# Kernel tuning notes

Hardware: AMD Instinct MI355X
Metric: run time of the kernel (lower is better)

## Reference

```python
import jax, jax.numpy as jnp
import numpy as np

N_ATOMS = 512
HEADS = 3
D1 = 16   # embedding_size1
D2 = 8    # embedding_size2
L1 = 32   # linear_size1
L2 = 16   # linear_size2
EPS = 1e-5


def _bn(x, gamma, beta):
    # PyG BatchNorm in training mode: batch statistics over nodes
    mu = x.mean(0)
    var = x.var(0)
    return (x - mu) * jax.lax.rsqrt(var + EPS) * gamma + beta


def setup_inputs() -> dict:
    key = jax.random.key(0)
    ks = jax.random.split(key, 24)
    N, E, C_in, C_out = 131072, 2097152, 32, 64
    s = lambda k, shape, fan: jax.random.normal(k, shape, jnp.float32) * (1.0 / np.sqrt(fan))
    inp = {
        "x": jax.random.normal(ks[0], (N, C_in), jnp.float32),
        "edge_index": jax.random.randint(ks[1], (2, E), 0, N, jnp.int64),
        # GATConv(in, 16, heads=3)
        "W_gat": s(ks[2], (C_in, HEADS * D1), C_in),
        "att_src": s(ks[3], (HEADS, D1), D1),
        "att_dst": s(ks[4], (HEADS, D1), D1),
        "b_gat": jnp.zeros((HEADS * D1,), jnp.float32),
        # head_transform1: Linear(48, 16)
        "W_ht": s(ks[5], (HEADS * D1, D1), HEADS * D1),
        "b_ht": jnp.zeros((D1,), jnp.float32),
        "g1": jnp.ones((D1,), jnp.float32),
        "be1": jnp.zeros((D1,), jnp.float32),
        # GCNConv(16, 8)
        "W_gcn": s(ks[6], (D1, D2), D1),
        "b_gcn": jnp.zeros((D2,), jnp.float32),
        "g2": jnp.ones((D2,), jnp.float32),
        "be2": jnp.zeros((D2,), jnp.float32),
        # dense head
        "W1": s(ks[7], (D2 * N_ATOMS, L1), D2 * N_ATOMS),
        "b1": jnp.zeros((L1,), jnp.float32),
        "W2": s(ks[8], (L1, L2), L1),
        "b2": jnp.zeros((L2,), jnp.float32),
        "Wt": s(ks[9], (L2, C_out), L2),
        "bt": jnp.zeros((C_out,), jnp.float32),
        "Wmu": s(ks[10], (C_out, C_out), C_out),
        "bmu": jnp.zeros((C_out,), jnp.float32),
        "Wls": s(ks[11], (C_out, C_out), C_out),
        "bls": jnp.zeros((C_out,), jnp.float32),
    }
    return inp


def _forward(x, edge_index, W_gat, att_src, att_dst, b_gat, W_ht, b_ht, g1, be1,
             W_gcn, b_gcn, g2, be2, W1, b1, W2, b2, Wt, bt, Wmu, bmu, Wls, bls):
    N = x.shape[0]
    loop = jnp.arange(N, dtype=edge_index.dtype)
    ei = jnp.concatenate([edge_index, jnp.stack([loop, loop])], axis=1)  # add self loops
    src, dst = ei[0], ei[1]

    # --- GATConv(in_channels, 16, heads=3) ---
    h = (x @ W_gat).reshape(N, HEADS, D1)                    # [N,H,D1]
    a_src = (h * att_src).sum(-1)                            # [N,H]
    a_dst = (h * att_dst).sum(-1)                            # [N,H]
    e = jax.nn.leaky_relu(a_src[src] + a_dst[dst], 0.2)      # [E',H]
    m = jax.ops.segment_max(e, dst, num_segments=N)          # per-target softmax
    w = jnp.exp(e - m[dst])
    z = jax.ops.segment_sum(w, dst, num_segments=N)
    alpha = w / z[dst]                                       # self-loops => z > 0
    msg = h[src] * alpha[:, :, None]                         # [E',H,D1]
    out = jax.ops.segment_sum(msg, dst, num_segments=N)
    out = out.reshape(N, HEADS * D1) + b_gat                 # concat heads + bias

    # head transform + BN1
    out = _bn(out @ W_ht + b_ht, g1, be1)                    # [N,16]

    # --- GCNConv(16, 8) with symmetric normalization ---
    deg = jax.ops.segment_sum(jnp.ones_like(dst, jnp.float32), dst, num_segments=N)
    dinv = jax.lax.rsqrt(deg)                                # deg >= 1 (self loops)
    norm = dinv[src] * dinv[dst]                             # [E']
    xw = out @ W_gcn                                         # [N,8]
    out = jax.ops.segment_sum(xw[src] * norm[:, None], dst, num_segments=N) + b_gcn
    out = _bn(out, g2, be2)                                  # [N,8]

    # --- per-graph dense head ---
    B = N // N_ATOMS
    out = out.reshape(B, N_ATOMS * D2)                       # flatten each graph
    out = jax.nn.leaky_relu(out @ W1 + b1)                   # [B,32]
    out = jax.nn.leaky_relu(out @ W2 + b2)                   # [B,16]
    out = jax.nn.leaky_relu(out @ Wt + bt)                   # [B,out]
    mu = out @ Wmu + bmu
    logstd = out @ Wls + bls
    return mu, logstd


def reference(x, edge_index, W_gat, att_src, att_dst, b_gat, W_ht, b_ht, g1, be1,
              W_gcn, b_gcn, g2, be2, W1, b1, W2, b2, Wt, bt, Wmu, bmu, Wls, bls):
    return _forward(x, edge_index, W_gat, att_src, att_dst, b_gat, W_ht, b_ht, g1, be1,
                    W_gcn, b_gcn, g2, be2, W1, b1, W2, b2, Wt, bt, Wmu, bmu, Wls, bls)
```

## Files before the change

### kernel.cpp

```cpp
#include <hip/hip_runtime.h>
#include <hip/hip_bf16.h>
#include <cstddef>

#define TPB 256
#define TPB_BIN 1024
#define NPB 512
#define BSH 9
#define CHUNK 8192

typedef unsigned int u32;

__device__ __forceinline__ float lrelu(float v, float s){ return v > 0.f ? v : s*v; }

__device__ __forceinline__ unsigned short bf16_rne(float f){
    u32 u = __float_as_uint(f);
    u += 0x7FFFu + ((u >> 16) & 1u);
    return (unsigned short)(u >> 16);
}
__device__ __forceinline__ float bf_lo(u32 w){ return __uint_as_float(w << 16); }
__device__ __forceinline__ float bf_hi(u32 w){ return __uint_as_float(w & 0xFFFF0000u); }

__global__ __launch_bounds__(TPB) void k1_embed(
    const float* __restrict__ x, const float* __restrict__ Wg,
    const float* __restrict__ atts, const float* __restrict__ attd,
    u32* __restrict__ hrow, float4* __restrict__ a_dst4, int N)
{
    __shared__ float Ws[32*48];
    __shared__ float As[48], Ad[48];
    for (int i = threadIdx.x; i < 32*48; i += TPB) Ws[i] = Wg[i];
    if (threadIdx.x < 48){ As[threadIdx.x] = atts[threadIdx.x]; Ad[threadIdx.x] = attd[threadIdx.x]; }
    __syncthreads();
    int n = blockIdx.x*TPB + threadIdx.x;
    if (n >= N) return;
    float xr[32];
    const float4* xp = (const float4*)(x + (size_t)n*32);
    #pragma unroll
    for (int i=0;i<8;i++){ float4 v = xp[i]; xr[4*i+0]=v.x; xr[4*i+1]=v.y; xr[4*i+2]=v.z; xr[4*i+3]=v.w; }
    float hv[48];
    #pragma unroll 4
    for (int j=0;j<48;j++){
        float acc = 0.f;
        #pragma unroll
        for (int i=0;i<32;i++) acc = fmaf(xr[i], Ws[i*48+j], acc);
        hv[j] = acc;
    }
    float asv[3], adv[3];
    #pragma unroll
    for (int hh=0;hh<3;hh++){
        float s0=0.f, s1=0.f;
        #pragma unroll
        for (int d=0;d<16;d++){ s0 = fmaf(hv[hh*16+d], As[hh*16+d], s0); s1 = fmaf(hv[hh*16+d], Ad[hh*16+d], s1); }
        asv[hh]=s0; adv[hh]=s1;
    }
    u32 w[24];
    #pragma unroll
    for (int q=0;q<12;q++){
        w[2*q]   = (u32)bf16_rne(hv[4*q+0]) | ((u32)bf16_rne(hv[4*q+1]) << 16);
        w[2*q+1] = (u32)bf16_rne(hv[4*q+2]) | ((u32)bf16_rne(hv[4*q+3]) << 16);
    }
    uint4* hp4 = (uint4*)(hrow + (size_t)n*32);
    hp4[0] = make_uint4(__float_as_uint(asv[0]), __float_as_uint(asv[1]), __float_as_uint(asv[2]), 0u);
    #pragma unroll
    for (int i=0;i<6;i++) hp4[1+i] = make_uint4(w[4*i],w[4*i+1],w[4*i+2],w[4*i+3]);
    hp4[7] = make_uint4(0u,0u,0u,0u);
    a_dst4[n] = make_float4(adv[0],adv[1],adv[2],0.f);
}

__global__ __launch_bounds__(TPB_BIN) void k_bin1(
    const int* __restrict__ ei, u32* __restrict__ staging,
    int* __restrict__ chunk_off, int* __restrict__ chunk_cnt,
    int* __restrict__ btot_pad, int E)
{
    __shared__ uint2 stash[CHUNK];
    __shared__ int lcnt[256], lcur[256];
    int t = threadIdx.x;
    int blockStart = blockIdx.x * CHUNK;
    int len = E - blockStart; if (len > CHUNK) len = CHUNK; if (len < 0) len = 0;
    if (t < 256) lcnt[t] = 0;
    __syncthreads();
    for (int i = t; i < len; i += TPB_BIN){
        int s = ei[blockStart + i];
        int d = ei[E + blockStart + i];
        stash[i] = make_uint2((unsigned)s, (unsigned)d);
        atomicAdd(&lcnt[d >> BSH], 1);
    }
    __syncthreads();
    if (t < 256){
        int myc = lcnt[t];
        atomicAdd(&btot_pad[t*16], myc);
        chunk_cnt[blockIdx.x*256 + t] = myc;
    }
    __syncthreads();
    if (t < 64){
        int v0=lcnt[4*t+0], v1=lcnt[4*t+1], v2=lcnt[4*t+2], v3=lcnt[4*t+3];
        int s = v0+v1+v2+v3, tot = s;
        #pragma unroll
        for (int off=1; off<64; off<<=1){ int xch = __shfl_up(s, off); if (t >= off) s += xch; }
        int base = s - tot;
        lcur[4*t+0]=base; lcur[4*t+1]=base+v0; lcur[4*t+2]=base+v0+v1; lcur[4*t+3]=base+v0+v1+v2;
    }
    __syncthreads();
    if (t < 256) chunk_off[blockIdx.x*256 + t] = lcur[t];
    __syncthreads();
    for (int i = t; i < len; i += TPB_BIN){
        uint2 e = stash[i];
        int b = (int)(e.y >> BSH);
        int pos = atomicAdd(&lcur[b], 1);
        staging[blockStart + pos] = e.x | ((e.y & (NPB-1u)) << 17);
    }
}

__global__ __launch_bounds__(TPB_BIN) void k_bin2(
    const u32* __restrict__ staging,
    const int* __restrict__ chunk_off, const int* __restrict__ chunk_cnt,
    const int* __restrict__ btot_pad, int* __restrict__ rowptr, int* __restrict__ cnt_g,
    int* __restrict__ csr_src, int NCB)
{
    __shared__ int co[256], cl[256];
    __shared__ int lcnt[NPB], lcur[NPB];
    __shared__ int cbs;
    int b = blockIdx.x, t = threadIdx.x;
    if (t < 256){
        co[t] = (t < NCB) ? chunk_off[t*256 + b] : 0;
        cl[t] = (t < NCB) ? chunk_cnt[t*256 + b] : 0;
    }
    if (t < NPB) lcnt[t] = 0;
    if (t < 64){
        int s = 0;
        for (int i=t; i<b; i+=64) s += btot_pad[i*16];
        #pragma unroll
        for (int off=32; off; off>>=1) s += __shfl_xor(s, off);
        if (t == 0) cbs = s;
    }
    __syncthreads();
    int cb = cbs;
    int wv = t >> 6, lane = t & 63;
    for (int c = wv; c < NCB; c += 16){
        int len = cl[c];
        size_t base = (size_t)c*CHUNK + co[c];
        for (int i = lane; i < len; i += 64){
            u32 val = staging[base + i];
            atomicAdd(&lcnt[(val>>17)&(NPB-1u)], 1);
        }
    }
    __syncthreads();
    if (t < 64){
        int v[8]; int ss = 0;
        #pragma unroll
        for (int k=0;k<8;k++){ v[k] = lcnt[8*t+k]; ss += v[k]; }
        int tot = ss;
        #pragma unroll
        for (int off=1; off<64; off<<=1){ int xch = __shfl_up(ss, off); if (t >= off) ss += xch; }
        int base = ss - tot;
        #pragma unroll
        for (int k=0;k<8;k++){ lcur[8*t+k] = base; base += v[k]; }
    }
    __syncthreads();
    if (t < NPB){ rowptr[b*NPB + t] = cb + lcur[t]; cnt_g[b*NPB + t] = lcnt[t]; }
    __syncthreads();
    for (int c = wv; c < NCB; c += 16){
        int len = cl[c];
        size_t base = (size_t)c*CHUNK + co[c];
        for (int i = lane; i < len; i += 64){
            u32 val = staging[base + i];
            int node = (int)((val>>17)&(NPB-1u));
            int pos = atomicAdd(&lcur[node],1);
            csr_src[cb+pos] = (int)(val & 0x1FFFFu);
        }
    }
}

__global__ __launch_bounds__(TPB) void k_gat(
    const int* __restrict__ rowptr, const int* __restrict__ cnt, const int* __restrict__ csr_src,
    const u32* __restrict__ hrow, const float* __restrict__ a_dstf,
    const float* __restrict__ b_gat,
    const float* __restrict__ W_ht, const float* __restrict__ b_ht,
    float* __restrict__ out_ht, float* __restrict__ part, int N, int cpx)
{
    __shared__ float Wh[768];
    __shared__ float bg[48], bh[16];
    __shared__ float gl[4][52];
    __shared__ float ls2[4][16];
    for (int i=threadIdx.x;i<768;i+=TPB) Wh[i]=W_ht[i];
    if (threadIdx.x<48) bg[threadIdx.x]=b_gat[threadIdx.x];
    if (threadIdx.x<16) bh[threadIdx.x]=b_ht[threadIdx.x];
    __syncthreads();
    int bid = blockIdx.x;
    int bid2 = (bid & 7)*cpx + (bid >> 3);
    int lane = threadIdx.x & 63;
    int wv = threadIdx.x >> 6;
    int n = bid2*4 + wv;

    int g = lane>>4, q = lane&15;
    int hq = (q < 12) ? (q >> 2) : (q - 12);
    if (q == 15) hq = 0;
    bool is_msg = (q < 12);
    bool is_z   = (q >= 12 && q < 15);

    float adh   = a_dstf[(size_t)n*4 + hq];
    float asn_h = __uint_as_float(hrow[(size_t)n*32 + hq]);
    float wself = __expf(lrelu(asn_h + adh, 0.2f));

    int rs = rowptr[n];
    int deg = cnt[n];

    float4 acc = make_float4(0.f,0.f,0.f,0.f);
    float zacc = 0.f;

    for (int base = 0; base < deg; base += 64){
        int m = deg - base; if (m > 64) m = 64;
        int idx = csr_src[rs + base + (lane < m ? lane : 0)];
        int niter = (m + 15) >> 4;
        for (int i = 0; i < niter; i++){
            int jj = g + (i << 4);
            int s0=__shfl(idx,jj), s1=__shfl(idx,jj+4), s2=__shfl(idx,jj+8), s3=__shfl(idx,jj+12);
            const u32* p0 = hrow + (size_t)s0*32;
            const u32* p1 = hrow + (size_t)s1*32;
            const u32* p2 = hrow + (size_t)s2*32;
            const u32* p3 = hrow + (size_t)s3*32;
            float av0=__uint_as_float(p0[hq]);
            float av1=__uint_as_float(p1[hq]);
            float av2=__uint_as_float(p2[hq]);
            float av3=__uint_as_float(p3[hq]);
            uint2 r0,r1,r2,r3;
            if (is_msg){
                r0=*(const uint2*)(p0+4+2*q); r1=*(const uint2*)(p1+4+2*q);
                r2=*(const uint2*)(p2+4+2*q); r3=*(const uint2*)(p3+4+2*q);
            }
            float w0 = (jj      < m) ? __expf(lrelu(av0+adh,0.2f)) : 0.f;
            float w1 = (jj + 4  < m) ? __expf(lrelu(av1+adh,0.2f)) : 0.f;
            float w2 = (jj + 8  < m) ? __expf(lrelu(av2+adh,0.2f)) : 0.f;
            float w3 = (jj + 12 < m) ? __expf(lrelu(av3+adh,0.2f)) : 0.f;
            if (is_msg){
                acc.x=fmaf(w0,bf_lo(r0.x),acc.x); acc.y=fmaf(w0,bf_hi(r0.x),acc.y);
                acc.z=fmaf(w0,bf_lo(r0.y),acc.z); acc.w=fmaf(w0,bf_hi(r0.y),acc.w);
                acc.x=fmaf(w1,bf_lo(r1.x),acc.x); acc.y=fmaf(w1,bf_hi(r1.x),acc.y);
                acc.z=fmaf(w1,bf_lo(r1.y),acc.z); acc.w=fmaf(w1,bf_hi(r1.y),acc.w);
                acc.x=fmaf(w2,bf_lo(r2.x),acc.x); acc.y=fmaf(w2,bf_hi(r2.x),acc.y);
                acc.z=fmaf(w2,bf_lo(r2.y),acc.z); acc.w=fmaf(w2,bf_hi(r2.y),acc.w);
                acc.x=fmaf(w3,bf_lo(r3.x),acc.x); acc.y=fmaf(w3,bf_hi(r3.x),acc.y);
                acc.z=fmaf(w3,bf_lo(r3.y),acc.z); acc.w=fmaf(w3,bf_hi(r3.y),acc.w);
            } else if (is_z){
                zacc += (w0+w1)+(w2+w3);
            }
        }
    }

    #pragma unroll
    for (int off=16; off<64; off<<=1){
        acc.x += __shfl_xor(acc.x, off); acc.y += __shfl_xor(acc.y, off);
        acc.z += __shfl_xor(acc.z, off); acc.w += __shfl_xor(acc.w, off);
        zacc  += __shfl_xor(zacc,  off);
    }
    float z_mine = __shfl(zacc, 12 + hq) + wself;

    if (g==0 && q<12){
        uint2 hs = *(const uint2*)(hrow + (size_t)n*32 + 4 + 2*q);
        float inv = 1.f / z_mine;
        float4 gq;
        gq.x = (acc.x + wself*bf_lo(hs.x))*inv + bg[4*q+0];
        gq.y = (acc.y + wself*bf_hi(hs.x))*inv + bg[4*q+1];
        gq.z = (acc.z + wself*bf_lo(hs.y))*inv + bg[4*q+2];
        gq.w = (acc.w + wself*bf_hi(hs.y))*inv + bg[4*q+3];
        *(float4*)&gl[wv][4*q] = gq;
    }
    __syncthreads();
    int j16 = lane & 15, pr = lane >> 4;
    float oacc = 0.f;
    const float* gv = &gl[wv][pr*12];
    #pragma unroll
    for (int k=0;k<12;k++) oacc = fmaf(gv[k], Wh[(pr*12+k)*16 + j16], oacc);
    oacc += __shfl_xor(oacc, 16);
    oacc += __shfl_xor(oacc, 32);
    float oval = oacc + bh[j16];
    if (lane < 16){
        out_ht[(size_t)n*16 + lane] = oval;
        ls2[wv][lane] = oval;
    }
    __syncthreads();
    int t = threadIdx.x;
    if (t < 16){
        float s=0.f, qd=0.f;
        #pragma unroll
        for (int w2=0;w2<4;w2++){ float v=ls2[w2][t]; s+=v; qd+=v*v; }
        part[(size_t)bid*32 + t] = s;
        part[(size_t)bid*32 + 16 + t] = qd;
    }
}

__global__ __launch_bounds__(TPB) void k_bnmid16(const float* __restrict__ part, float* __restrict__ part2)
{
    __shared__ float ls[8][32];
    int t = threadIdx.x, b = blockIdx.x;
    int col = t & 31, grp = t >> 5;
    float s = 0.f;
    #pragma unroll
    for (int i=0;i<16;i++){ int r = b*128 + grp*16 + i; s += part[(size_t)r*32 + col]; }
    ls[grp][col] = s; __syncthreads();
    if (t < 32){
        float a = 0.f;
        #pragma unroll
        for (int g=0; g<8; g++) a += ls[g][t];
        part2[(size_t)b*32 + t] = a;
    }
}

__global__ __launch_bounds__(TPB) void k_bnfin16(const float* __restrict__ part2, float* __restrict__ bn, int NB)
{
    __shared__ float ls[8][32];
    int t = threadIdx.x, col = t & 31, grp = t >> 5;
    float s = 0.f;
    for (int r=grp; r<NB; r+=8) s += part2[(size_t)r*32+col];
    ls[grp][col] = s; __syncthreads();
    if (t < 32){
        float a = 0.f;
        #pragma unroll
        for (int g=0; g<8; g++) a += ls[g][t];
        bn[t] = a;
    }
}

__global__ __launch_bounds__(TPB) void k_bnmid8(const float* __restrict__ part, float* __restrict__ part2)
{
    __shared__ float ls[16][16];
    int t = threadIdx.x, b = blockIdx.x;
    int col = t & 15, grp = t >> 4;
    float s = 0.f;
    #pragma unroll
    for (int i=0;i<8;i++){ int r = b*128 + grp + 16*i; s += part[(size_t)r*16 + col]; }
    ls[grp][col] = s; __syncthreads();
    if (t < 16){
        float a = 0.f;
        #pragma unroll
        for (int g=0; g<16; g++) a += ls[g][t];
        part2[(size_t)b*16 + t] = a;
    }
}

__global__ __launch_bounds__(TPB) void k_bnfin8(const float* __restrict__ part2, float* __restrict__ bn, int NB)
{
    __shared__ float ls[16][16];
    int t = threadIdx.x, col = t & 15, grp = t >> 4;
    float s = 0.f;
    for (int r=grp; r<NB; r+=16) s += part2[(size_t)r*16+col];
    ls[grp][col] = s; __syncthreads();
    if (t < 16){
        float a = 0.f;
        #pragma unroll
        for (int g=0; g<16; g++) a += ls[g][t];
        bn[t] = a;
    }
}

__global__ __launch_bounds__(TPB) void k5_bn1_gcnmm(
    const float* __restrict__ out_ht, const float* __restrict__ bn,
    const float* __restrict__ g1, const float* __restrict__ be1,
    const float* __restrict__ W_gcn, const int* __restrict__ cnt,
    float* __restrict__ dinv, uint4* __restrict__ xws, int N)
{
    __shared__ float sc[16], sh[16], Wg[128];
    int t = threadIdx.x;
    if (t < 16){
        float mu  = bn[t]/(float)N;
        float var = bn[16+t]/(float)N - mu*mu;
        float s = rsqrtf(var+1e-5f)*g1[t];
        sc[t]=s; sh[t]=be1[t]-mu*s;
    }
    if (t < 128) Wg[t] = W_gcn[t];
    __syncthreads();
    int n = blockIdx.x*TPB + t;
    if (n >= N) return;
    float v[16];
    const float4* ip = (const float4*)(out_ht + (size_t)n*16);
    #pragma unroll
    for (int q=0;q<4;q++){
        float4 vv = ip[q];
        v[4*q+0]=vv.x*sc[4*q+0]+sh[4*q+0];
        v[4*q+1]=vv.y*sc[4*q+1]+sh[4*q+1];
        v[4*q+2]=vv.z*sc[4*q+2]+sh[4*q+2];
        v[4*q+3]=vv.w*sc[4*q+3]+sh[4*q+3];
    }
    float dv = rsqrtf((float)(cnt[n]+1));
    float o[8];
    #pragma unroll
    for (int k=0;k<8;k++){
        float acc=0.f;
        #pragma unroll
        for (int j=0;j<16;j++) acc = fmaf(v[j], Wg[j*8+k], acc);
        o[k]=acc*dv;
    }
    u32 w0 = (u32)bf16_rne(o[0]) | ((u32)bf16_rne(o[1])<<16);
    u32 w1 = (u32)bf16_rne(o[2]) | ((u32)bf16_rne(o[3])<<16);
    u32 w2 = (u32)bf16_rne(o[4]) | ((u32)bf16_rne(o[5])<<16);
    u32 w3 = (u32)bf16_rne(o[6]) | ((u32)bf16_rne(o[7])<<16);
    xws[n] = make_uint4(w0,w1,w2,w3);
    dinv[n] = dv;
}

__global__ __launch_bounds__(TPB) void k_gcn(
    const int* __restrict__ rowptr, const int* __restrict__ cnt, const int* __restrict__ csr_src,
    const float* __restrict__ dinv, const uint4* __restrict__ xws,
    const float* __restrict__ b_gcn, float* __restrict__ gout, float* __restrict__ part, int N, int cpx)
{
    __shared__ float ls[16][16];
    int bid = blockIdx.x;
    int bid2 = (bid & 7)*cpx + (bid >> 3);
    int t = threadIdx.x;
    int node = bid2*16 + (t >> 4);
    int sub  = t & 15;
    int grp  = t >> 4;
    float val[8];
    #pragma unroll
    for (int k=0;k<8;k++) val[k]=0.f;
    if (node < N){
        int rs = rowptr[node], re = rs + cnt[node];
        float a0=0.f,a1=0.f,a2=0.f,a3=0.f,a4=0.f,a5=0.f,a6=0.f,a7=0.f;
        for (int j=rs+sub; j<re; j+=16){
            int s = csr_src[j];
            uint4 r = xws[s];
            a0 += bf_lo(r.x); a1 += bf_hi(r.x);
            a2 += bf_lo(r.y); a3 += bf_hi(r.y);
            a4 += bf_lo(r.z); a5 += bf_hi(r.z);
            a6 += bf_lo(r.w); a7 += bf_hi(r.w);
        }
        #pragma unroll
        for (int off=1; off<16; off<<=1){
            a0 += __shfl_xor(a0, off); a1 += __shfl_xor(a1, off);
            a2 += __shfl_xor(a2, off); a3 += __shfl_xor(a3, off);
            a4 += __shfl_xor(a4, off); a5 += __shfl_xor(a5, off);
            a6 += __shfl_xor(a6, off); a7 += __shfl_xor(a7, off);
        }
        if (sub == 0){
            uint4 r = xws[node];
            a0 += bf_lo(r.x); a1 += bf_hi(r.x);
            a2 += bf_lo(r.y); a3 += bf_hi(r.y);
            a4 += bf_lo(r.z); a5 += bf_hi(r.z);
            a6 += bf_lo(r.w); a7 += bf_hi(r.w);
            float dd = dinv[node];
            val[0]=fmaf(dd,a0,b_gcn[0]); val[1]=fmaf(dd,a1,b_gcn[1]);
            val[2]=fmaf(dd,a2,b_gcn[2]); val[3]=fmaf(dd,a3,b_gcn[3]);
            val[4]=fmaf(dd,a4,b_gcn[4]); val[5]=fmaf(dd,a5,b_gcn[5]);
            val[6]=fmaf(dd,a6,b_gcn[6]); val[7]=fmaf(dd,a7,b_gcn[7]);
            float4* op = (float4*)(gout + (size_t)node*8);
            op[0] = make_float4(val[0],val[1],val[2],val[3]);
            op[1] = make_float4(val[4],val[5],val[6],val[7]);
        }
    }
    if (sub == 0){
        #pragma unroll
        for (int k=0;k<8;k++){ ls[grp][k] = val[k]; ls[grp][8+k] = val[k]*val[k]; }
    }
    __syncthreads();
    if (t < 16){
        float s = 0.f;
        #pragma unroll
        for (int g2=0; g2<16; g2++) s += ls[g2][t];
        part[(size_t)bid*16 + t] = s;
    }
}

__global__ __launch_bounds__(TPB) void k8_head(
    const float* __restrict__ gcn, const float* __restrict__ bn2,
    const float* __restrict__ g2, const float* __restrict__ be2,
    const float* __restrict__ W1, const float* __restrict__ b1,
    const float* __restrict__ W2, const float* __restrict__ b2,
    const float* __restrict__ Wt, const float* __restrict__ bt,
    const float* __restrict__ Wmu, const float* __restrict__ bmu,
    const float* __restrict__ Wls, const float* __restrict__ bls,
    float* __restrict__ out, int N, int B)
{
    __shared__ float v[4096];
    __shared__ float red[8][32];
    __shared__ float y1[32], y2[16], y3[64];
    int b = blockIdx.x, t = threadIdx.x;
    float sc[8], sh[8];
    #pragma unroll
    for (int k=0;k<8;k++){
        float mu  = bn2[k]/(float)N;
        float var = bn2[8+k]/(float)N - mu*mu;
        float s = rsqrtf(var+1e-5f)*g2[k];
        sc[k]=s; sh[k]=be2[k]-mu*s;
    }
    const float* src = gcn + (size_t)b*4096;
    for (int i=t;i<4096;i+=TPB){ int k=i&7; v[i]=src[i]*sc[k]+sh[k]; }
    __syncthreads();
    int j = t & 31, c = t >> 5;
    float p = 0.f;
    int base = c*512;
    for (int i=0;i<512;i++) p = fmaf(v[base+i], W1[(size_t)(base+i)*32+j], p);
    red[c][j] = p;
    __syncthreads();
    if (t < 32){
        float a = b1[t];
        #pragma unroll
        for (int cc=0;cc<8;cc++) a += red[cc][t];
        y1[t] = lrelu(a, 0.01f);
    }
    __syncthreads();
    if (t < 16){
        float a = b2[t];
        #pragma unroll
        for (int i=0;i<32;i++) a = fmaf(y1[i], W2[i*16+t], a);
        y2[t] = lrelu(a, 0.01f);
    }
    __syncthreads();
    if (t < 64){
        float a = bt[t];
        #pragma unroll
        for (int i=0;i<16;i++) a = fmaf(y2[i], Wt[i*64+t], a);
        y3[t] = lrelu(a, 0.01f);
    }
    __syncthreads();
    if (t < 64){
        float amu = bmu[t], als = bls[t];
        #pragma unroll
        for (int i=0;i<64;i++){ amu = fmaf(y3[i], Wmu[i*64+t], amu); als = fmaf(y3[i], Wls[i*64+t], als); }
        out[(size_t)b*64 + t] = amu;
        out[(size_t)B*64 + (size_t)b*64 + t] = als;
    }
}

extern "C" void kernel_launch(void* const* d_in, const int* in_sizes, int n_in,
                              void* d_out, int out_size, void* d_ws, size_t ws_size,
                              hipStream_t stream)
{
    const float* x     = (const float*)d_in[0];
    const int*   ei    = (const int*)  d_in[1];
    const float* W_gat = (const float*)d_in[2];
    const float* atts  = (const float*)d_in[3];
    const float* attd  = (const float*)d_in[4];
    const float* b_gat = (const float*)d_in[5];
    const float* W_ht  = (const float*)d_in[6];
    const float* b_ht  = (const float*)d_in[7];
    const float* g1    = (const float*)d_in[8];
    const float* be1   = (const float*)d_in[9];
    const float* W_gcn = (const float*)d_in[10];
    const float* b_gcn = (const float*)d_in[11];
    const float* g2    = (const float*)d_in[12];
    const float* be2   = (const float*)d_in[13];
    const float* W1    = (const float*)d_in[14];
    const float* b1    = (const float*)d_in[15];
    const float* W2    = (const float*)d_in[16];
    const float* b2    = (const float*)d_in[17];
    const float* Wt    = (const float*)d_in[18];
    const float* bt    = (const float*)d_in[19];
    const float* Wmu   = (const float*)d_in[20];
    const float* bmu   = (const float*)d_in[21];
    const float* Wls   = (const float*)d_in[22];
    const float* bls   = (const float*)d_in[23];
    float* out = (float*)d_out;

    const int N = in_sizes[0] / 32;
    const int E = in_sizes[1] / 2;
    const int B = N / 512;
    const int NBUCK = N / NPB;
    const int NCB = (E + CHUNK - 1) / CHUNK;

    char* wsb = (char*)d_ws;
    size_t off = 0;
    auto alloc = [&](size_t bytes){ void* p = wsb + off; off += (bytes + 255) & ~(size_t)255; return p; };
    char*   hreg    = (char*)  alloc((size_t)N*128);
    float*  out_ht  = (float*) alloc((size_t)N*16*4);
    float4* a_dst4  = (float4*)alloc((size_t)N*16);
    float*  dinv    = (float*) alloc((size_t)N*4);
    float*  bn      = (float*) alloc(64*4);
    int*    cnt     = (int*)   alloc((size_t)N*4);
    int*    rowptr  = (int*)   alloc((size_t)N*4);
    float*  part    = (float*) alloc((size_t)(N/4)*32*4);
    float*  part2   = (float*) alloc(8192*4);
    int*    csr_src = (int*)   alloc((size_t)E*4);
    u32*    staging = (u32*)   alloc((size_t)NCB*CHUNK*4);
    int*    chunk_off = (int*) alloc((size_t)NCB*256*4);
    int*    chunk_cnt = (int*) alloc((size_t)NCB*256*4);
    int*    btot_pad  = (int*) alloc((size_t)NBUCK*16*4);
    u32*    hrow    = (u32*)hreg;
    uint4*  xws     = (uint4*)hreg;
    float*  gout    = (float*)(hreg + (size_t)N*16);

    hipMemsetAsync(btot_pad, 0, (size_t)NBUCK*16*4, stream);

    dim3 tb(TPB);
    dim3 tbb(TPB_BIN);
    int gbN = (N+TPB-1)/TPB;
    int nbGat = N/4;
    int nbGcn = N/16;

    k_bin1   <<<NCB,   tbb, 0, stream>>>(ei, staging, chunk_off, chunk_cnt, btot_pad, E);
    k_bin2   <<<NBUCK, tbb, 0, stream>>>(staging, chunk_off, chunk_cnt, btot_pad, rowptr, cnt, csr_src, NCB);
    k1_embed <<<gbN,   tb, 0, stream>>>(x, W_gat, atts, attd, hrow, a_dst4, N);
    k_gat    <<<nbGat, tb, 0, stream>>>(rowptr, cnt, csr_src, hrow, (const float*)a_dst4,
                                        b_gat, W_ht, b_ht, out_ht, part, N, nbGat/8);
    k_bnmid16 <<<256,  tb, 0, stream>>>(part, part2);
    k_bnfin16 <<<1,    tb, 0, stream>>>(part2, bn, 256);
    k5_bn1_gcnmm<<<gbN, tb, 0, stream>>>(out_ht, bn, g1, be1, W_gcn, cnt, dinv, xws, N);
    k_gcn    <<<nbGcn, tb, 0, stream>>>(rowptr, cnt, csr_src, dinv, xws, b_gcn, gout, part, N, nbGcn/8);
    k_bnmid8 <<<64,    tb, 0, stream>>>(part, part2);
    k_bnfin8 <<<1,     tb, 0, stream>>>(part2, bn+32, 64);
    k8_head  <<<B,     tb, 0, stream>>>(gout, bn+32, g2, be2, W1, b1, W2, b2, Wt, bt, Wmu, bmu, Wls, bls, out, N, B);
}
```

Measured before the change: 213.1 us.

## Pack a_dst into hrow padding, peel GAT tail loop, fuse BN finalize kernels

The destination attention scores now go into the unused padding slot of each hrow record, so the separate a_dst buffer is neither written nor read. The GAT edge loop is split into full 16-edge iterations without bounds predicates plus a single masked tail. The two single-block BN finalize kernels are removed and their reductions are redone redundantly inside every block of the following kernels. This cuts two launches and some memory traffic, at the cost of each block re-reading the small partial-sum arrays.

```diff
diff --git a/kernel.cpp b/kernel.cpp
--- a/kernel.cpp
+++ b/kernel.cpp
@@ -23,7 +23,7 @@
 __global__ __launch_bounds__(TPB) void k1_embed(
     const float* __restrict__ x, const float* __restrict__ Wg,
     const float* __restrict__ atts, const float* __restrict__ attd,
-    u32* __restrict__ hrow, float4* __restrict__ a_dst4, int N)
+    u32* __restrict__ hrow, int N)
 {
     __shared__ float Ws[32*48];
     __shared__ float As[48], Ad[48];
@@ -62,8 +62,7 @@
     hp4[0] = make_uint4(__float_as_uint(asv[0]), __float_as_uint(asv[1]), __float_as_uint(asv[2]), 0u);
     #pragma unroll
     for (int i=0;i<6;i++) hp4[1+i] = make_uint4(w[4*i],w[4*i+1],w[4*i+2],w[4*i+3]);
-    hp4[7] = make_uint4(0u,0u,0u,0u);
-    a_dst4[n] = make_float4(adv[0],adv[1],adv[2],0.f);
+    hp4[7] = make_uint4(__float_as_uint(adv[0]), __float_as_uint(adv[1]), __float_as_uint(adv[2]), 0u);
 }
 
 __global__ __launch_bounds__(TPB_BIN) void k_bin1(
@@ -172,7 +171,7 @@
 
 __global__ __launch_bounds__(TPB) void k_gat(
     const int* __restrict__ rowptr, const int* __restrict__ cnt, const int* __restrict__ csr_src,
-    const u32* __restrict__ hrow, const float* __restrict__ a_dstf,
+    const u32* __restrict__ hrow,
     const float* __restrict__ b_gat,
     const float* __restrict__ W_ht, const float* __restrict__ b_ht,
     float* __restrict__ out_ht, float* __restrict__ part, int N, int cpx)
@@ -197,7 +196,7 @@
     bool is_msg = (q < 12);
     bool is_z   = (q >= 12 && q < 15);
 
-    float adh   = a_dstf[(size_t)n*4 + hq];
+    float adh   = __uint_as_float(hrow[(size_t)n*32 + 28 + hq]);
     float asn_h = __uint_as_float(hrow[(size_t)n*32 + hq]);
     float wself = __expf(lrelu(asn_h + adh, 0.2f));
 
@@ -210,9 +209,42 @@
     for (int base = 0; base < deg; base += 64){
         int m = deg - base; if (m > 64) m = 64;
         int idx = csr_src[rs + base + (lane < m ? lane : 0)];
-        int niter = (m + 15) >> 4;
-        for (int i = 0; i < niter; i++){
+        int nfull = m >> 4;
+        for (int i = 0; i < nfull; i++){
             int jj = g + (i << 4);
+            int s0=__shfl(idx,jj), s1=__shfl(idx,jj+4), s2=__shfl(idx,jj+8), s3=__shfl(idx,jj+12);
+            const u32* p0 = hrow + (size_t)s0*32;
+            const u32* p1 = hrow + (size_t)s1*32;
+            const u32* p2 = hrow + (size_t)s2*32;
+            const u32* p3 = hrow + (size_t)s3*32;
+            float av0=__uint_as_float(p0[hq]);
+            float av1=__uint_as_float(p1[hq]);
+            float av2=__uint_as_float(p2[hq]);
+            float av3=__uint_as_float(p3[hq]);
+            uint2 r0,r1,r2,r3;
+            if (is_msg){
+                r0=*(const uint2*)(p0+4+2*q); r1=*(const uint2*)(p1+4+2*q);
+                r2=*(const uint2*)(p2+4+2*q); r3=*(const uint2*)(p3+4+2*q);
+            }
+            float w0 = __expf(lrelu(av0+adh,0.2f));
+            float w1 = __expf(lrelu(av1+adh,0.2f));
+            float w2 = __expf(lrelu(av2+adh,0.2f));
+            float w3 = __expf(lrelu(av3+adh,0.2f));
+            if (is_msg){
+                acc.x=fmaf(w0,bf_lo(r0.x),acc.x); acc.y=fmaf(w0,bf_hi(r0.x),acc.y);
+                acc.z=fmaf(w0,bf_lo(r0.y),acc.z); acc.w=fmaf(w0,bf_hi(r0.y),acc.w);
+                acc.x=fmaf(w1,bf_lo(r1.x),acc.x); acc.y=fmaf(w1,bf_hi(r1.x),acc.y);
+                acc.z=fmaf(w1,bf_lo(r1.y),acc.z); acc.w=fmaf(w1,bf_hi(r1.y),acc.w);
+                acc.x=fmaf(w2,bf_lo(r2.x),acc.x); acc.y=fmaf(w2,bf_hi(r2.x),acc.y);
+                acc.z=fmaf(w2,bf_lo(r2.y),acc.z); acc.w=fmaf(w2,bf_hi(r2.y),acc.w);
+                acc.x=fmaf(w3,bf_lo(r3.x),acc.x); acc.y=fmaf(w3,bf_hi(r3.x),acc.y);
+                acc.z=fmaf(w3,bf_lo(r3.y),acc.z); acc.w=fmaf(w3,bf_hi(r3.y),acc.w);
+            } else if (is_z){
+                zacc += (w0+w1)+(w2+w3);
+            }
+        }
+        if (m & 15){
+            int jj = g + (nfull << 4);
             int s0=__shfl(idx,jj), s1=__shfl(idx,jj+4), s2=__shfl(idx,jj+8), s3=__shfl(idx,jj+12);
             const u32* p0 = hrow + (size_t)s0*32;
             const u32* p1 = hrow + (size_t)s1*32;
@@ -305,21 +337,6 @@
     }
 }
 
-__global__ __launch_bounds__(TPB) void k_bnfin16(const float* __restrict__ part2, float* __restrict__ bn, int NB)
-{
-    __shared__ float ls[8][32];
-    int t = threadIdx.x, col = t & 31, grp = t >> 5;
-    float s = 0.f;
-    for (int r=grp; r<NB; r+=8) s += part2[(size_t)r*32+col];
-    ls[grp][col] = s; __syncthreads();
-    if (t < 32){
-        float a = 0.f;
-        #pragma unroll
-        for (int g=0; g<8; g++) a += ls[g][t];
-        bn[t] = a;
-    }
-}
-
 __global__ __launch_bounds__(TPB) void k_bnmid8(const float* __restrict__ part, float* __restrict__ part2)
 {
     __shared__ float ls[16][16];
@@ -337,36 +354,38 @@
     }
 }
 
-__global__ __launch_bounds__(TPB) void k_bnfin8(const float* __restrict__ part2, float* __restrict__ bn, int NB)
-{
-    __shared__ float ls[16][16];
-    int t = threadIdx.x, col = t & 15, grp = t >> 4;
-    float s = 0.f;
-    for (int r=grp; r<NB; r+=16) s += part2[(size_t)r*16+col];
-    ls[grp][col] = s; __syncthreads();
-    if (t < 16){
-        float a = 0.f;
-        #pragma unroll
-        for (int g=0; g<16; g++) a += ls[g][t];
-        bn[t] = a;
-    }
-}
-
 __global__ __launch_bounds__(TPB) void k5_bn1_gcnmm(
-    const float* __restrict__ out_ht, const float* __restrict__ bn,
+    const float* __restrict__ out_ht, const float* __restrict__ part2,
     const float* __restrict__ g1, const float* __restrict__ be1,
     const float* __restrict__ W_gcn, const int* __restrict__ cnt,
     float* __restrict__ dinv, uint4* __restrict__ xws, int N)
 {
+    __shared__ float ls[8][32];
+    __shared__ float bnv[32];
     __shared__ float sc[16], sh[16], Wg[128];
     int t = threadIdx.x;
+    {
+        int col = t & 31, grp = t >> 5;
+        float s = 0.f;
+        #pragma unroll
+        for (int i=0;i<32;i++) s += part2[(size_t)(grp + 8*i)*32 + col];
+        ls[grp][col] = s;
+    }
+    if (t < 128) Wg[t] = W_gcn[t];
+    __syncthreads();
+    if (t < 32){
+        float a = 0.f;
+        #pragma unroll
+        for (int g=0; g<8; g++) a += ls[g][t];
+        bnv[t] = a;
+    }
+    __syncthreads();
     if (t < 16){
-        float mu  = bn[t]/(float)N;
-        float var = bn[16+t]/(float)N - mu*mu;
+        float mu  = bnv[t]/(float)N;
+        float var = bnv[16+t]/(float)N - mu*mu;
         float s = rsqrtf(var+1e-5f)*g1[t];
         sc[t]=s; sh[t]=be1[t]-mu*s;
     }
-    if (t < 128) Wg[t] = W_gcn[t];
     __syncthreads();
     int n = blockIdx.x*TPB + t;
     if (n >= N) return;
@@ -460,7 +479,7 @@
 }
 
 __global__ __launch_bounds__(TPB) void k8_head(
-    const float* __restrict__ gcn, const float* __restrict__ bn2,
+    const float* __restrict__ gcn, const float* __restrict__ part2,
     const float* __restrict__ g2, const float* __restrict__ be2,
     const float* __restrict__ W1, const float* __restrict__ b1,
     const float* __restrict__ W2, const float* __restrict__ b2,
@@ -471,13 +490,30 @@
 {
     __shared__ float v[4096];
     __shared__ float red[8][32];
+    __shared__ float ls8[16][16];
+    __shared__ float bnv[16];
     __shared__ float y1[32], y2[16], y3[64];
     int b = blockIdx.x, t = threadIdx.x;
+    {
+        int col = t & 15, grp = t >> 4;
+        float s = 0.f;
+        #pragma unroll
+        for (int i=0;i<4;i++) s += part2[(size_t)(grp + 16*i)*16 + col];
+        ls8[grp][col] = s;
+    }
+    __syncthreads();
+    if (t < 16){
+        float a = 0.f;
+        #pragma unroll
+        for (int g=0; g<16; g++) a += ls8[g][t];
+        bnv[t] = a;
+    }
+    __syncthreads();
     float sc[8], sh[8];
     #pragma unroll
     for (int k=0;k<8;k++){
-        float mu  = bn2[k]/(float)N;
-        float var = bn2[8+k]/(float)N - mu*mu;
+        float mu  = bnv[k]/(float)N;
+        float var = bnv[8+k]/(float)N - mu*mu;
         float s = rsqrtf(var+1e-5f)*g2[k];
         sc[k]=s; sh[k]=be2[k]-mu*s;
     }
@@ -561,9 +597,7 @@
     auto alloc = [&](size_t bytes){ void* p = wsb + off; off += (bytes + 255) & ~(size_t)255; return p; };
     char*   hreg    = (char*)  alloc((size_t)N*128);
     float*  out_ht  = (float*) alloc((size_t)N*16*4);
-    float4* a_dst4  = (float4*)alloc((size_t)N*16);
     float*  dinv    = (float*) alloc((size_t)N*4);
-    float*  bn      = (float*) alloc(64*4);
     int*    cnt     = (int*)   alloc((size_t)N*4);
     int*    rowptr  = (int*)   alloc((size_t)N*4);
     float*  part    = (float*) alloc((size_t)(N/4)*32*4);
@@ -587,14 +621,12 @@
 
     k_bin1   <<<NCB,   tbb, 0, stream>>>(ei, staging, chunk_off, chunk_cnt, btot_pad, E);
     k_bin2   <<<NBUCK, tbb, 0, stream>>>(staging, chunk_off, chunk_cnt, btot_pad, rowptr, cnt, csr_src, NCB);
-    k1_embed <<<gbN,   tb, 0, stream>>>(x, W_gat, atts, attd, hrow, a_dst4, N);
-    k_gat    <<<nbGat, tb, 0, stream>>>(rowptr, cnt, csr_src, hrow, (const float*)a_dst4,
+    k1_embed <<<gbN,   tb, 0, stream>>>(x, W_gat, atts, attd, hrow, N);
+    k_gat    <<<nbGat, tb, 0, stream>>>(rowptr, cnt, csr_src, hrow,
                                         b_gat, W_ht, b_ht, out_ht, part, N, nbGat/8);
     k_bnmid16 <<<256,  tb, 0, stream>>>(part, part2);
-    k_bnfin16 <<<1,    tb, 0, stream>>>(part2, bn, 256);
-    k5_bn1_gcnmm<<<gbN, tb, 0, stream>>>(out_ht, bn, g1, be1, W_gcn, cnt, dinv, xws, N);
+    k5_bn1_gcnmm<<<gbN, tb, 0, stream>>>(out_ht, part2, g1, be1, W_gcn, cnt, dinv, xws, N);
     k_gcn    <<<nbGcn, tb, 0, stream>>>(rowptr, cnt, csr_src, dinv, xws, b_gcn, gout, part, N, nbGcn/8);
     k_bnmid8 <<<64,    tb, 0, stream>>>(part, part2);
-    k_bnfin8 <<<1,     tb, 0, stream>>>(part2, bn+32, 64);
-    k8_head  <<<B,     tb, 0, stream>>>(gout, bn+32, g2, be2, W1, b1, W2, b2, Wt, bt, Wmu, bmu, Wls, bls, out, N, B);
-}
+    k8_head  <<<B,     tb, 0, stream>>>(gout, part2, g2, be2, W1, b1, W2, b2, Wt, bt, Wmu, bmu, Wls, bls, out, N, B);
+}
```

After: 210.7 us. About the same (-1.1%).
